# Kernel tuning notes

Measured on AMD Instinct MI355X. Metric: run time of the kernel, lower is better.

The kernel has to match this reference:

```python
import jax, jax.numpy as jnp
import numpy as np

NUM_TREES = 100
TREE_DEPTH = 5
INPUT_DIM = 256
NUM_CLASSES = 64
BATCH = 8192
NUM_NODES = 2 ** TREE_DEPTH - 1   # 31 decision nodes per tree
NUM_LEAVES = 2 ** TREE_DEPTH      # 32 leaves per tree


def setup_inputs() -> dict:
    key = jax.random.key(0)
    k_x, k_w, k_b, k_l = jax.random.split(key, 4)
    x = jax.random.normal(k_x, (BATCH, INPUT_DIM), dtype=jnp.float32)
    # stacked per-tree decision-node params (torch.randn init)
    node_w = jax.random.normal(k_w, (NUM_TREES, NUM_NODES, INPUT_DIM), dtype=jnp.float32)
    node_b = jax.random.normal(k_b, (NUM_TREES, NUM_NODES), dtype=jnp.float32)
    leaves = jax.random.normal(k_l, (NUM_TREES, NUM_LEAVES, NUM_CLASSES), dtype=jnp.float32)
    return {"x": x, "node_w": node_w, "node_b": node_b, "leaves": leaves}


def reference(x, node_w, node_b, leaves):
    # x: [B, D]; node_w: [T, Nn, D]; node_b: [T, Nn]; leaves: [T, Nl, C]
    T = node_w.shape[0]
    B = x.shape[0]
    depth = int(np.log2(leaves.shape[1]))
    idx = jnp.zeros((T, B), dtype=jnp.int32)
    for _ in range(depth):  # small fixed depth loop
        # gather each sample's routing node per tree: [T, B, D] and [T, B]
        w_g = jnp.take_along_axis(node_w, idx[:, :, None], axis=1)
        b_g = jnp.take_along_axis(node_b, idx, axis=1)
        decisions = jax.nn.sigmoid(jnp.einsum('tbd,bd->tb', w_g, x) + b_g)
        idx = 2 * idx + (decisions <= 0.5).astype(jnp.int32)
    # leaf gather: [T, B, C], then forest average over trees -> [B, C]
    tree_preds = jnp.take_along_axis(leaves, idx[:, :, None], axis=1)
    return jnp.mean(tree_preds, axis=0)
```

## Files before the change

kernel.cpp:

```cpp
#include <hip/hip_runtime.h>


typedef __bf16 bf16;
typedef __attribute__((ext_vector_type(8))) __bf16 bf16x8;
typedef __attribute__((ext_vector_type(4))) float f32x4;

#define NTREES 100
#define NB     8192
#define ND     256
#define NNODES 31
#define NLEAF  32
#define NCLS   64
#define TAU    2.0e-3f
#define FQCAP  32

__global__ __launch_bounds__(256, 3) void forest_all(
    const float* __restrict__ x,
    const float* __restrict__ wf,
    const float* __restrict__ bias,
    unsigned char* __restrict__ idxb)
{
    __shared__ char lds[50176];
    bf16*  Wh  = (bf16*)lds;
    bf16*  Wl  = (bf16*)(lds + 16384);
    float* scr = (float*)(lds + 32768);
    __shared__ int fcnt;
    __shared__ unsigned short fitems[FQCAP];
    __shared__ unsigned char  fres[FQCAP];

    const int tid  = threadIdx.x;
    const int wave = tid >> 6;
    const int lane = tid & 63;
    const int m    = lane & 15;
    const int q    = lane >> 4;
    const int tg   = blockIdx.x;
    const int mg   = blockIdx.y;

    if (tid == 0) fcnt = 0;

    float biasv[4];
#pragma unroll
    for (int ni = 0; ni < 4; ++ni)
        biasv[ni] = bias[(size_t)(tg * 4 + ni) * NNODES + m];

    f32x4 acc[4][4];
#pragma unroll
    for (int mi = 0; mi < 4; ++mi)
#pragma unroll
        for (int ni = 0; ni < 4; ++ni)
            acc[mi][ni] = (f32x4){0.f, 0.f, 0.f, 0.f};

    const float* xbase[4];
#pragma unroll
    for (int mi = 0; mi < 4; ++mi)
        xbase[mi] = x + (size_t)(mg * 256 + wave * 64 + mi * 16 + m) * ND + q * 8;

    const int srow = wave * 16 + (lane & 15);
    const float* wrow = wf + ((size_t)(tg * 4 + (srow >> 4)) * NNODES + (srow & 15)) * ND;

#pragma unroll
    for (int kc = 0; kc < 2; ++kc) {
        __syncthreads();
#pragma unroll
        for (int it = 0; it < 4; ++it) {
            int c = (lane >> 4) + it * 4;
            const float* src = wrow + kc * 128 + c * 8;
            float4 f0 = *(const float4*)(src);
            float4 f1 = *(const float4*)(src + 4);
            float fv[8] = {f0.x, f0.y, f0.z, f0.w, f1.x, f1.y, f1.z, f1.w};
            bf16x8 h8, l8;
#pragma unroll
            for (int e = 0; e < 8; ++e) {
                bf16 h = (bf16)fv[e];
                h8[e] = h;
                l8[e] = (bf16)(fv[e] - (float)h);
            }
            int swz = c ^ (srow & 7);
            *(bf16x8*)(Wh + srow * 128 + swz * 8) = h8;
            *(bf16x8*)(Wl + srow * 128 + swz * 8) = l8;
        }
        __syncthreads();

        float4 ca[4], cb[4], na[4], nb2[4];
#pragma unroll
        for (int mi = 0; mi < 4; ++mi) {
            const float* p = xbase[mi] + kc * 128;
            ca[mi] = *(const float4*)p;
            cb[mi] = *(const float4*)(p + 4);
        }
#pragma unroll
        for (int kk = 0; kk < 4; ++kk) {
            if (kk < 3) {
#pragma unroll
                for (int mi = 0; mi < 4; ++mi) {
                    const float* p = xbase[mi] + kc * 128 + (kk + 1) * 32;
                    na[mi]  = *(const float4*)p;
                    nb2[mi] = *(const float4*)(p + 4);
                }
            }
            bf16x8 ah[4], al[4];
#pragma unroll
            for (int mi = 0; mi < 4; ++mi) {
                float fv[8] = {ca[mi].x, ca[mi].y, ca[mi].z, ca[mi].w,
                               cb[mi].x, cb[mi].y, cb[mi].z, cb[mi].w};
#pragma unroll
                for (int e = 0; e < 8; ++e) {
                    bf16 h = (bf16)fv[e];
                    ah[mi][e] = h;
                    al[mi][e] = (bf16)(fv[e] - (float)h);
                }
            }
#pragma unroll
            for (int ni = 0; ni < 4; ++ni) {
                const int n    = ni * 16 + m;
                const int cidx = (4 * kk + q) ^ (m & 7);
                bf16x8 bh = *(const bf16x8*)(Wh + n * 128 + cidx * 8);
                bf16x8 bl = *(const bf16x8*)(Wl + n * 128 + cidx * 8);
#pragma unroll
                for (int mi = 0; mi < 4; ++mi) {
                    acc[mi][ni] = __builtin_amdgcn_mfma_f32_16x16x32_bf16(al[mi], bh, acc[mi][ni], 0, 0, 0);
                    acc[mi][ni] = __builtin_amdgcn_mfma_f32_16x16x32_bf16(ah[mi], bl, acc[mi][ni], 0, 0, 0);
                    acc[mi][ni] = __builtin_amdgcn_mfma_f32_16x16x32_bf16(ah[mi], bh, acc[mi][ni], 0, 0, 0);
                }
            }
#pragma unroll
            for (int mi = 0; mi < 4; ++mi) { ca[mi] = na[mi]; cb[mi] = nb2[mi]; }
        }
    }

    float* ws_ = scr + wave * (64 * 17);
    const int s_l = wave * 64 + lane;
    const int sg  = mg * 256 + s_l;
    unsigned int pk = 0;
#pragma unroll
    for (int ni = 0; ni < 4; ++ni) {
#pragma unroll
        for (int mi = 0; mi < 4; ++mi)
#pragma unroll
            for (int r = 0; r < 4; ++r)
                ws_[(mi * 16 + q * 4 + r) * 17 + m] = acc[mi][ni][r] + biasv[ni];
        __syncthreads();
        int node = 0;
        float mn = 1e30f;
#pragma unroll
        for (int lvl = 0; lvl < 5; ++lvl) {
            float z = ws_[lane * 17 + node];
            mn = fminf(mn, fabsf(z));
            node = 2 * node + (z <= 0.0f ? 1 : 0);
        }
        pk |= (unsigned)node << (8 * ni);
        if (mn < TAU) {
            int p = atomicAdd(&fcnt, 1);
            if (p < FQCAP) fitems[p] = (unsigned short)((s_l << 2) | ni);
        }
        __syncthreads();
    }

    int cnt = fcnt;
    if (cnt > FQCAP) cnt = FQCAP;
    for (int i = wave; i < cnt; i += 4) {
        int it  = fitems[i];
        int sl2 = it >> 2, ni = it & 3;
        int t   = tg * 4 + ni;
        const float* xr = x + (size_t)(mg * 256 + sl2) * ND;
        float4 xv = *(const float4*)(xr + lane * 4);
        int node = 0;
        for (int lvl = 0; lvl < 5; ++lvl) {
            const float* wr = wf + ((size_t)t * NNODES + node) * ND;
            float4 wv = *(const float4*)(wr + lane * 4);
            double zz = (double)xv.x * wv.x + (double)xv.y * wv.y
                      + (double)xv.z * wv.z + (double)xv.w * wv.w;
#pragma unroll
            for (int o = 32; o > 0; o >>= 1) zz += __shfl_xor(zz, o);
            zz += (double)bias[t * NNODES + node];
            node = 2 * node + (zz <= 0.0 ? 1 : 0);
        }
        if (lane == 0) fres[i] = (unsigned char)node;
    }
    __syncthreads();

    for (int i = 0; i < cnt; ++i) {
        int it = fitems[i];
        if ((it >> 2) == s_l) {
            int ni = it & 3;
            pk = (pk & ~(255u << (8 * ni))) | ((unsigned)fres[i] << (8 * ni));
        }
    }
    *(unsigned int*)(idxb + (size_t)sg * NTREES + tg * 4) = pk;
}

__global__ void leaf_gather(const unsigned char* __restrict__ idxb,
                            const float* __restrict__ leaves,
                            float* __restrict__ out) {
    const int wave = threadIdx.x >> 6;
    const int lane = threadIdx.x & 63;
    const int s = blockIdx.x * 4 + wave;
    unsigned int rw = 0;
    if (lane < 25) rw = *(const unsigned int*)(idxb + (size_t)s * NTREES + lane * 4);
    float acc = 0.f;
#pragma unroll 10
    for (int t = 0; t < NTREES; ++t) {
        unsigned int wrd = __shfl(rw, t >> 2);
        int li = (wrd >> ((t & 3) * 8)) & 255;
        acc += leaves[((size_t)t * NLEAF + li) * NCLS + lane];
    }
    out[(size_t)s * NCLS + lane] = acc * 0.01f;
}

extern "C" void kernel_launch(void* const* d_in, const int* in_sizes, int n_in,
                              void* d_out, int out_size, void* d_ws, size_t ws_size,
                              hipStream_t stream) {
    const float* x  = (const float*)d_in[0];
    const float* nw = (const float*)d_in[1];
    const float* nb = (const float*)d_in[2];
    const float* lv = (const float*)d_in[3];
    float* out = (float*)d_out;

    unsigned char* idxb = (unsigned char*)d_ws;
    if (ws_size < (size_t)819200) return;

    forest_all<<<dim3(NTREES / 4, NB / 256), 256, 0, stream>>>(x, nw, nb, idxb);
    leaf_gather<<<NB / 4, 256, 0, stream>>>(idxb, lv, out);
}
```

Before: 119.2 us.

## Precompute bf16 hi/lo splits of x and weights in a prep kernel

Adds a prep kernel that converts x and node weights once into bf16 high/low pairs, storing them in MFMA-friendly fragment and swizzled LDS image layouts in workspace. The main kernel then loads those fragments and copies the weight image straight into LDS, so no block repeats the conversion. Previously each of the 25 tree-group blocks re-split the same x rows. The score scratch now reuses the weight LDS region, shrinking LDS use and dropping per-iteration barriers. The cost is an extra launch plus extra global traffic for the split copies.

```diff
diff --git a/kernel.cpp b/kernel.cpp
--- a/kernel.cpp
+++ b/kernel.cpp
@@ -14,19 +14,62 @@
 #define TAU    2.0e-3f
 #define FQCAP  32
 
+__global__ void prep(const float* __restrict__ x, const float* __restrict__ wf,
+                     bf16* __restrict__ xh, bf16* __restrict__ xl,
+                     bf16* __restrict__ wimg) {
+    if (blockIdx.x < 1024) {
+        int i = blockIdx.x * 256 + threadIdx.x;
+        int m  = i & 15;
+        int dq = (i >> 4) & 31;
+        int g  = i >> 9;
+        const float* src = x + (size_t)(g * 16 + m) * ND + dq * 8;
+        bf16x8 h8, l8;
+#pragma unroll
+        for (int e = 0; e < 8; ++e) {
+            float f = src[e];
+            bf16 h = (bf16)f;
+            h8[e] = h;
+            l8[e] = (bf16)(f - (float)h);
+        }
+        *(bf16x8*)(xh + (size_t)i * 8) = h8;
+        *(bf16x8*)(xl + (size_t)i * 8) = l8;
+    } else {
+        int i = (blockIdx.x - 1024) * 256 + threadIdx.x;
+        int oct = i & 31;
+        int row = (i >> 5) & 63;
+        int tg  = i >> 11;
+        int tree = tg * 4 + (row >> 4), node = row & 15;
+        const float* src = wf + ((size_t)tree * NNODES + node) * ND + oct * 8;
+        bf16x8 h8, l8;
+#pragma unroll
+        for (int e = 0; e < 8; ++e) {
+            float f = src[e];
+            bf16 h = (bf16)f;
+            h8[e] = h;
+            l8[e] = (bf16)(f - (float)h);
+        }
+        int kc = oct >> 4, c = oct & 15, cp = c ^ (row & 7);
+        size_t b = (size_t)tg * 32768 + (size_t)kc * 16384 + row * 128 + cp * 8;
+        *(bf16x8*)(wimg + b)        = h8;
+        *(bf16x8*)(wimg + b + 8192) = l8;
+    }
+}
+
 __global__ __launch_bounds__(256, 3) void forest_all(
+    const bf16* __restrict__ xh, const bf16* __restrict__ xl,
+    const bf16* __restrict__ wimg,
     const float* __restrict__ x,
     const float* __restrict__ wf,
     const float* __restrict__ bias,
     unsigned char* __restrict__ idxb)
 {
-    __shared__ char lds[50176];
-    bf16*  Wh  = (bf16*)lds;
-    bf16*  Wl  = (bf16*)(lds + 16384);
-    float* scr = (float*)(lds + 32768);
+    __shared__ char lds[32768];
     __shared__ int fcnt;
     __shared__ unsigned short fitems[FQCAP];
     __shared__ unsigned char  fres[FQCAP];
+    bf16*  Wh  = (bf16*)lds;
+    bf16*  Wl  = (bf16*)(lds + 16384);
+    float* scr = (float*)lds;
 
     const int tid  = threadIdx.x;
     const int wave = tid >> 6;
@@ -50,65 +93,32 @@
         for (int ni = 0; ni < 4; ++ni)
             acc[mi][ni] = (f32x4){0.f, 0.f, 0.f, 0.f};
 
-    const float* xbase[4];
+    size_t abase[4];
 #pragma unroll
     for (int mi = 0; mi < 4; ++mi)
-        xbase[mi] = x + (size_t)(mg * 256 + wave * 64 + mi * 16 + m) * ND + q * 8;
-
-    const int srow = wave * 16 + (lane & 15);
-    const float* wrow = wf + ((size_t)(tg * 4 + (srow >> 4)) * NNODES + (srow & 15)) * ND;
+        abase[mi] = (size_t)(mg * 16 + wave * 4 + mi) * 4096 + lane * 8;
+
+    const bf16* wsrc = wimg + (size_t)tg * 32768;
 
 #pragma unroll
     for (int kc = 0; kc < 2; ++kc) {
         __syncthreads();
 #pragma unroll
-        for (int it = 0; it < 4; ++it) {
-            int c = (lane >> 4) + it * 4;
-            const float* src = wrow + kc * 128 + c * 8;
-            float4 f0 = *(const float4*)(src);
-            float4 f1 = *(const float4*)(src + 4);
-            float fv[8] = {f0.x, f0.y, f0.z, f0.w, f1.x, f1.y, f1.z, f1.w};
-            bf16x8 h8, l8;
-#pragma unroll
-            for (int e = 0; e < 8; ++e) {
-                bf16 h = (bf16)fv[e];
-                h8[e] = h;
-                l8[e] = (bf16)(fv[e] - (float)h);
-            }
-            int swz = c ^ (srow & 7);
-            *(bf16x8*)(Wh + srow * 128 + swz * 8) = h8;
-            *(bf16x8*)(Wl + srow * 128 + swz * 8) = l8;
+        for (int j = 0; j < 8; ++j) {
+            int idx = j * 256 + tid;
+            *(bf16x8*)(lds + idx * 16) =
+                *(const bf16x8*)(wsrc + (size_t)kc * 16384 + idx * 8);
         }
         __syncthreads();
 
-        float4 ca[4], cb[4], na[4], nb2[4];
-#pragma unroll
-        for (int mi = 0; mi < 4; ++mi) {
-            const float* p = xbase[mi] + kc * 128;
-            ca[mi] = *(const float4*)p;
-            cb[mi] = *(const float4*)(p + 4);
-        }
 #pragma unroll
         for (int kk = 0; kk < 4; ++kk) {
-            if (kk < 3) {
-#pragma unroll
-                for (int mi = 0; mi < 4; ++mi) {
-                    const float* p = xbase[mi] + kc * 128 + (kk + 1) * 32;
-                    na[mi]  = *(const float4*)p;
-                    nb2[mi] = *(const float4*)(p + 4);
-                }
-            }
             bf16x8 ah[4], al[4];
 #pragma unroll
             for (int mi = 0; mi < 4; ++mi) {
-                float fv[8] = {ca[mi].x, ca[mi].y, ca[mi].z, ca[mi].w,
-                               cb[mi].x, cb[mi].y, cb[mi].z, cb[mi].w};
-#pragma unroll
-                for (int e = 0; e < 8; ++e) {
-                    bf16 h = (bf16)fv[e];
-                    ah[mi][e] = h;
-                    al[mi][e] = (bf16)(fv[e] - (float)h);
-                }
+                size_t off = abase[mi] + (size_t)(kc * 16 + kk * 4) * 128;
+                ah[mi] = *(const bf16x8*)(xh + off);
+                al[mi] = *(const bf16x8*)(xl + off);
             }
 #pragma unroll
             for (int ni = 0; ni < 4; ++ni) {
@@ -123,12 +133,11 @@
                     acc[mi][ni] = __builtin_amdgcn_mfma_f32_16x16x32_bf16(ah[mi], bh, acc[mi][ni], 0, 0, 0);
                 }
             }
-#pragma unroll
-            for (int mi = 0; mi < 4; ++mi) { ca[mi] = na[mi]; cb[mi] = nb2[mi]; }
-        }
-    }
-
-    float* ws_ = scr + wave * (64 * 17);
+        }
+    }
+    __syncthreads();
+
+    float* ws_ = scr + wave * 1088;
     const int s_l = wave * 64 + lane;
     const int sg  = mg * 256 + s_l;
     unsigned int pk = 0;
@@ -139,7 +148,6 @@
 #pragma unroll
             for (int r = 0; r < 4; ++r)
                 ws_[(mi * 16 + q * 4 + r) * 17 + m] = acc[mi][ni][r] + biasv[ni];
-        __syncthreads();
         int node = 0;
         float mn = 1e30f;
 #pragma unroll
@@ -153,8 +161,8 @@
             int p = atomicAdd(&fcnt, 1);
             if (p < FQCAP) fitems[p] = (unsigned short)((s_l << 2) | ni);
         }
-        __syncthreads();
-    }
+    }
+    __syncthreads();
 
     int cnt = fcnt;
     if (cnt > FQCAP) cnt = FQCAP;
@@ -216,9 +224,15 @@
     const float* lv = (const float*)d_in[3];
     float* out = (float*)d_out;
 
-    unsigned char* idxb = (unsigned char*)d_ws;
-    if (ws_size < (size_t)819200) return;
-
-    forest_all<<<dim3(NTREES / 4, NB / 256), 256, 0, stream>>>(x, nw, nb, idxb);
+    char* ws = (char*)d_ws;
+    bf16* xh   = (bf16*)(ws + 0);
+    bf16* xl   = (bf16*)(ws + 4194304);
+    bf16* wimg = (bf16*)(ws + 8388608);
+    unsigned char* idxb = (unsigned char*)(ws + 10027008);
+    if (ws_size < (size_t)10846208) return;
+
+    prep<<<1224, 256, 0, stream>>>(x, nw, xh, xl, wimg);
+    forest_all<<<dim3(NTREES / 4, NB / 256), 256, 0, stream>>>(
+        xh, xl, wimg, x, nw, nb, idxb);
     leaf_gather<<<NB / 4, 256, 0, stream>>>(idxb, lv, out);
 }
```

After: 111.6 us. 1.07x faster.
